# Kernel optimization log

Hardware: AMD Instinct MI355X
Metric: run time of the kernel (lower is better)

## Reference

```python
import jax, jax.numpy as jnp
import numpy as np

HEADS = 8
DIM_HEAD = 64


def setup_inputs() -> dict:
    key = jax.random.key(0)
    k1, k2, k3 = jax.random.split(key, 3)
    dim = 512
    hidden = HEADS * DIM_HEAD  # 512
    x = jax.random.normal(k1, (16, dim, 64, 64), dtype=jnp.float32)
    # 1x1 convs expressed as dense matrices (out_ch, in_ch)
    w_qkv = jax.random.normal(k2, (3 * hidden, dim), dtype=jnp.float32) * (1.0 / np.sqrt(dim))
    w_out = jax.random.normal(k3, (dim, hidden), dtype=jnp.float32) * (1.0 / np.sqrt(hidden))
    b_out = jnp.zeros((dim,), dtype=jnp.float32)
    return {"x": x, "w_qkv": w_qkv, "w_out": w_out, "b_out": b_out}


def reference(x, w_qkv, w_out, b_out):
    b, c, h, w = x.shape
    hw = h * w
    # 1x1 conv == channel matmul: (b, 3*hidden, hw)
    xf = x.reshape(b, c, hw)
    qkv = jnp.einsum('oc,bcn->bon', w_qkv, xf)
    # split into q,k,v each (b, heads, dim_head, hw)
    qkv = qkv.reshape(b, 3, HEADS, DIM_HEAD, hw)
    q, k, v = qkv[:, 0], qkv[:, 1], qkv[:, 2]
    k = jax.nn.softmax(k, axis=-1)  # softmax over spatial dim
    # context: (b, heads, dim_head, dim_head)
    context = jnp.einsum('bhcn,bhdn->bhcd', k, v)
    # out: context^T @ q -> (b, heads, dim_head, hw)
    out = jnp.einsum('bhcd,bhcn->bhdn', context, q)
    out = out.reshape(b, HEADS * DIM_HEAD, h, w)
    # to_out 1x1 conv with bias
    outf = out.reshape(b, HEADS * DIM_HEAD, hw)
    y = jnp.einsum('oc,bcn->bon', w_out, outf) + b_out[None, :, None]
    return y.reshape(b, -1, h, w)
```

## Files before the change

kernel.cpp:

```cpp
#include <hip/hip_runtime.h>
#include <string.h>

typedef __bf16 bf16x8 __attribute__((ext_vector_type(8)));
typedef float f32x4 __attribute__((ext_vector_type(4)));
typedef unsigned short u16;
typedef u16 u16x8 __attribute__((ext_vector_type(8)));

#define NB 16
#define CD 512
#define NN 4096
#define O3 1536

__device__ __forceinline__ u16 f2bf(float f) {
    union { float f; unsigned int u; } v; v.f = f;
    unsigned int r = v.u + 0x7fffu + ((v.u >> 16) & 1u);
    return (u16)(r >> 16);
}
__device__ __forceinline__ float bf2f(u16 s) {
    union { unsigned int u; float f; } v; v.u = ((unsigned int)s) << 16;
    return v.f;
}

__device__ __forceinline__ void gl2lds16(const u16* g, u16* l) {
    __builtin_amdgcn_global_load_lds(
        (const void __attribute__((address_space(1)))*)g,
        (void __attribute__((address_space(3)))*)l,
        16, 0, 0);
}

__global__ void k_convert(const float* __restrict__ in, u16* __restrict__ out, int n) {
    int i = blockIdx.x * 256 + threadIdx.x;
    if (i < n) out[i] = f2bf(in[i]);
}

__global__ __launch_bounds__(256) void k_transpose_x(const float* __restrict__ x,
                                                     u16* __restrict__ xt) {
    __shared__ float tile[64][65];
    const int b = blockIdx.y;
    const int ntile = blockIdx.x & 63;
    const int ctile = blockIdx.x >> 6;
    const int t = threadIdx.x;
    const int r = t >> 2;
    const int q = t & 3;

    const float* xb = x + ((size_t)b * CD + ctile * 64 + r) * NN + ntile * 64;
#pragma unroll
    for (int j = 0; j < 4; ++j) {
        float4 v = *(const float4*)&xb[q * 16 + j * 4];
        tile[r][q * 16 + j * 4 + 0] = v.x;
        tile[r][q * 16 + j * 4 + 1] = v.y;
        tile[r][q * 16 + j * 4 + 2] = v.z;
        tile[r][q * 16 + j * 4 + 3] = v.w;
    }
    __syncthreads();
    u16* xtb = xt + ((size_t)b * NN + ntile * 64 + r) * CD + ctile * 64 + q * 16;
    u16x8 o0, o1;
#pragma unroll
    for (int j = 0; j < 8; ++j) {
        o0[j] = f2bf(tile[q * 16 + j][r]);
        o1[j] = f2bf(tile[q * 16 + 8 + j][r]);
    }
    *(u16x8*)&xtb[0] = o0;
    *(u16x8*)&xtb[8] = o1;
}

__global__ __launch_bounds__(256, 2) void k_gemm1(
        const u16* __restrict__ A, const u16* __restrict__ Bt,
        u16* __restrict__ qt, u16* __restrict__ kbuf, u16* __restrict__ vbuf) {
    __shared__ __align__(16) u16 As[128 * 64];
    __shared__ __align__(16) u16 Bs[128 * 64];
    const int t = threadIdx.x;
    const int gid = blockIdx.x;
    const int xcd = gid & 7;
    const int j = gid >> 3;
    const int ot = j % 12;
    const int bn = (j / 12) * 8 + xcd;
    const int b = bn >> 5;
    const int nt = bn & 31;

    const int lane = t & 63, w = t >> 6;
    const int l15 = lane & 15, quad = lane >> 4;
    const int wm = (w >> 1) * 64, wn = (w & 1) * 64;
    const int srow = t >> 3;
    const int kc = (t & 7) * 8;

    const u16* Ab = A + (size_t)(ot * 128) * CD;
    const u16* Bb = Bt + (size_t)b * NN * CD + (size_t)(nt * 128) * CD;

    f32x4 acc[4][4] = {};

    for (int k0 = 0; k0 < CD; k0 += 64) {
        __syncthreads();
        gl2lds16(Ab + (size_t)(srow     ) * CD + k0 + kc, &As[t * 8]);
        gl2lds16(Ab + (size_t)(srow + 32) * CD + k0 + kc, &As[2048 + t * 8]);
        gl2lds16(Ab + (size_t)(srow + 64) * CD + k0 + kc, &As[4096 + t * 8]);
        gl2lds16(Ab + (size_t)(srow + 96) * CD + k0 + kc, &As[6144 + t * 8]);
        gl2lds16(Bb + (size_t)(srow     ) * CD + k0 + kc, &Bs[t * 8]);
        gl2lds16(Bb + (size_t)(srow + 32) * CD + k0 + kc, &Bs[2048 + t * 8]);
        gl2lds16(Bb + (size_t)(srow + 64) * CD + k0 + kc, &Bs[4096 + t * 8]);
        gl2lds16(Bb + (size_t)(srow + 96) * CD + k0 + kc, &Bs[6144 + t * 8]);
        __syncthreads();
#pragma unroll
        for (int h = 0; h < 2; ++h) {
            bf16x8 af[4], bfr[4];
#pragma unroll
            for (int mi = 0; mi < 4; ++mi)
                af[mi] = *(const bf16x8*)&As[(wm + mi * 16 + l15) * 64 + h * 32 + quad * 8];
#pragma unroll
            for (int ni = 0; ni < 4; ++ni)
                bfr[ni] = *(const bf16x8*)&Bs[(wn + ni * 16 + l15) * 64 + h * 32 + quad * 8];
#pragma unroll
            for (int mi = 0; mi < 4; ++mi)
#pragma unroll
                for (int ni = 0; ni < 4; ++ni)
                    acc[mi][ni] = __builtin_amdgcn_mfma_f32_16x16x32_bf16(
                        af[mi], bfr[ni], acc[mi][ni], 0, 0, 0);
        }
    }

    const int sec = ot >> 2;
    const int lrowbase = ot * 128 - sec * 512;
#pragma unroll
    for (int mi = 0; mi < 4; ++mi) {
        int lr = lrowbase + wm + mi * 16 + quad * 4;
#pragma unroll
        for (int ni = 0; ni < 4; ++ni) {
            int nc = nt * 128 + wn + ni * 16 + l15;
            if (sec == 0) {
                ushort4 pk;
                pk.x = f2bf(acc[mi][ni][0]); pk.y = f2bf(acc[mi][ni][1]);
                pk.z = f2bf(acc[mi][ni][2]); pk.w = f2bf(acc[mi][ni][3]);
                *(ushort4*)&qt[((size_t)b * NN + nc) * CD + lr] = pk;
            } else {
                u16* dst = (sec == 1) ? kbuf : vbuf;
#pragma unroll
                for (int r = 0; r < 4; ++r)
                    dst[((size_t)(b * 512 + lr + r)) * NN + nc] = f2bf(acc[mi][ni][r]);
            }
        }
    }
}

__global__ __launch_bounds__(256) void k_ctx(const u16* __restrict__ kbuf,
                                             const u16* __restrict__ vbuf,
                                             float* __restrict__ ctxT,
                                             float* __restrict__ lsum) {
    const int bh = blockIdx.y;
    const int chunk = blockIdx.x;
    const int t = threadIdx.x, lane = t & 63, w = t >> 6;
    const int l15 = lane & 15, quad = lane >> 4;
    const int cb = w * 16;

    const u16* krow = kbuf + (size_t)(bh * 64 + cb + l15) * NN;
    const u16* vb   = vbuf + (size_t)bh * 64 * NN;

    f32x4 acc[4] = {};
    float ls = 0.f;
    for (int i = 0; i < 32; ++i) {
        int n0 = chunk * 1024 + i * 32 + quad * 8;
        u16x8 ku = *(const u16x8*)&krow[n0];
        u16x8 afu;
#pragma unroll
        for (int jj = 0; jj < 8; ++jj) {
            float ev = __expf(fminf(bf2f(ku[jj]), 30.f));
            ls += ev;
            afu[jj] = f2bf(ev);
        }
        bf16x8 af = __builtin_bit_cast(bf16x8, afu);
#pragma unroll
        for (int di = 0; di < 4; ++di) {
            bf16x8 bfv = *(const bf16x8*)&vb[(size_t)(di * 16 + l15) * NN + n0];
            acc[di] = __builtin_amdgcn_mfma_f32_16x16x32_bf16(af, bfv, acc[di], 0, 0, 0);
        }
    }
    ls += __shfl_xor(ls, 16);
    ls += __shfl_xor(ls, 32);
    if (quad == 0) atomicAdd(&lsum[(size_t)bh * 64 + cb + l15], ls);

    const int c = cb + quad * 4;
#pragma unroll
    for (int di = 0; di < 4; ++di) {
        int d = di * 16 + l15;
#pragma unroll
        for (int r = 0; r < 4; ++r)
            atomicAdd(&ctxT[((size_t)bh * 64 + d) * 64 + c + r], acc[di][r]);
    }
}

__global__ __launch_bounds__(256) void k_weff(const float* __restrict__ wout,
                                              const float* __restrict__ ctxT,
                                              const float* __restrict__ lsum,
                                              u16* __restrict__ weff) {
    int idx = blockIdx.x * 256 + threadIdx.x;
    int b = idx >> 18;
    int o = (idx >> 9) & 511;
    int hc = idx & 511;
    int h = hc >> 6, c = hc & 63;
    const float* wr = wout + o * 512 + h * 64;
    const float* cr = ctxT + ((size_t)b * 8 + h) * 4096 + c;
    float s = 0.f;
#pragma unroll
    for (int d = 0; d < 64; ++d) s += wr[d] * cr[d * 64];
    s *= 1.0f / lsum[((size_t)b * 8 + h) * 64 + c];
    weff[idx] = f2bf(s);
}

__global__ __launch_bounds__(256, 2) void k_gemm2(
        const u16* __restrict__ weff, const u16* __restrict__ qt,
        const float* __restrict__ bout, float* __restrict__ y) {
    __shared__ __align__(16) u16 As[128 * 64];
    __shared__ __align__(16) u16 Bs[128 * 64];
    const int t = threadIdx.x;
    const int gid = blockIdx.x;
    const int xcd = gid & 7;
    const int j = gid >> 3;
    const int ot = j & 3;
    const int bn = (j >> 2) * 8 + xcd;
    const int b = bn >> 5;
    const int nt = bn & 31;

    const int lane = t & 63, w = t >> 6;
    const int l15 = lane & 15, quad = lane >> 4;
    const int wm = (w >> 1) * 64, wn = (w & 1) * 64;
    const int srow = t >> 3;
    const int kc = (t & 7) * 8;

    const u16* Ab = weff + (size_t)b * 512 * 512 + (size_t)(ot * 128) * CD;
    const u16* Bb = qt + (size_t)b * NN * CD + (size_t)(nt * 128) * CD;

    f32x4 acc[4][4] = {};

    for (int k0 = 0; k0 < CD; k0 += 64) {
        __syncthreads();
        gl2lds16(Ab + (size_t)(srow     ) * CD + k0 + kc, &As[t * 8]);
        gl2lds16(Ab + (size_t)(srow + 32) * CD + k0 + kc, &As[2048 + t * 8]);
        gl2lds16(Ab + (size_t)(srow + 64) * CD + k0 + kc, &As[4096 + t * 8]);
        gl2lds16(Ab + (size_t)(srow + 96) * CD + k0 + kc, &As[6144 + t * 8]);
        gl2lds16(Bb + (size_t)(srow     ) * CD + k0 + kc, &Bs[t * 8]);
        gl2lds16(Bb + (size_t)(srow + 32) * CD + k0 + kc, &Bs[2048 + t * 8]);
        gl2lds16(Bb + (size_t)(srow + 64) * CD + k0 + kc, &Bs[4096 + t * 8]);
        gl2lds16(Bb + (size_t)(srow + 96) * CD + k0 + kc, &Bs[6144 + t * 8]);
        __syncthreads();
#pragma unroll
        for (int h = 0; h < 2; ++h) {
            bf16x8 af[4], bfr[4];
#pragma unroll
            for (int mi = 0; mi < 4; ++mi)
                af[mi] = *(const bf16x8*)&As[(wm + mi * 16 + l15) * 64 + h * 32 + quad * 8];
#pragma unroll
            for (int ni = 0; ni < 4; ++ni)
                bfr[ni] = *(const bf16x8*)&Bs[(wn + ni * 16 + l15) * 64 + h * 32 + quad * 8];
#pragma unroll
            for (int mi = 0; mi < 4; ++mi)
#pragma unroll
                for (int ni = 0; ni < 4; ++ni)
                    acc[mi][ni] = __builtin_amdgcn_mfma_f32_16x16x32_bf16(
                        af[mi], bfr[ni], acc[mi][ni], 0, 0, 0);
        }
    }

#pragma unroll
    for (int mi = 0; mi < 4; ++mi) {
        int o = ot * 128 + wm + mi * 16 + quad * 4;
#pragma unroll
        for (int ni = 0; ni < 4; ++ni) {
            int nc = nt * 128 + wn + ni * 16 + l15;
#pragma unroll
            for (int r = 0; r < 4; ++r)
                y[((size_t)(b * 512 + o + r)) * NN + nc] = acc[mi][ni][r] + bout[o + r];
        }
    }
}

extern "C" void kernel_launch(void* const* d_in, const int* in_sizes, int n_in,
                              void* d_out, int out_size, void* d_ws, size_t ws_size,
                              hipStream_t stream) {
    const float* x    = (const float*)d_in[0];
    const float* wqkv = (const float*)d_in[1];
    const float* wout = (const float*)d_in[2];
    const float* bout = (const float*)d_in[3];
    float* y = (float*)d_out;

    char* ws = (char*)d_ws;
    u16*   xt   = (u16*)(ws);
    u16*   wqb  = (u16*)(ws + 67108864);
    u16*   qt   = (u16*)(ws + 68681728);
    u16*   kbuf = (u16*)(ws + 135790592);
    u16*   vbuf = (u16*)(ws + 202899456);
    float* ctxT = (float*)(ws + 270008320);
    float* lsum = (float*)(ws + 272105472);
    u16*   weff = (u16*)(ws + 272138240);

    hipMemsetAsync(ctxT, 0, 2097152 + 32768, stream);

    k_convert<<<(O3 * CD + 255) / 256, 256, 0, stream>>>(wqkv, wqb, O3 * CD);
    k_transpose_x<<<dim3(64 * 8, NB), 256, 0, stream>>>(x, xt);
    k_gemm1<<<12 * 32 * NB, 256, 0, stream>>>(wqb, xt, qt, kbuf, vbuf);
    k_ctx<<<dim3(4, NB * 8), 256, 0, stream>>>(kbuf, vbuf, ctxT, lsum);
    k_weff<<<(NB * 512 * 512) / 256, 256, 0, stream>>>(wout, ctxT, lsum, weff);
    k_gemm2<<<4 * 32 * NB, 256, 0, stream>>>(weff, qt, bout, y);
}
```

Measured before the change: 538.6 us.

## Rewrite both GEMMs as 256x256 tiles with double-buffered swizzled LDS pipeline

Both projection GEMMs move from 128x128 tiles with a single LDS buffer and two full syncs per k-step to a shared 256x256-tile core with 8 waves. The core double-buffers LDS, prefetches the next k-slices in quarter chunks interleaved with MFMA groups, XOR-swizzles the LDS layout to avoid bank conflicts, and raises wave priority during MFMA. The block-to-XCD mapping is also reworked for L2 locality. The aim is to hide global-load latency and cut LDS traffic per flop, at the cost of 128KB of LDS per block, more registers, and fragile hand-placed waitcnt and barrier logic.

```diff
diff --git a/kernel.cpp b/kernel.cpp
--- a/kernel.cpp
+++ b/kernel.cpp
@@ -64,78 +64,149 @@
     *(u16x8*)&xtb[8] = o1;
 }
 
-__global__ __launch_bounds__(256, 2) void k_gemm1(
+
+__device__ __forceinline__ void lda8(const u16* p, bf16x8 (&aa)[4][2],
+                                     int aoff, int sw0, int sw1) {
+#pragma unroll
+    for (int mi = 0; mi < 4; ++mi) {
+        aa[mi][0] = *(const bf16x8*)&p[aoff + mi * 1024 + sw0];
+        aa[mi][1] = *(const bf16x8*)&p[aoff + mi * 1024 + sw1];
+    }
+}
+
+__device__ __forceinline__ void ldb4(const u16* p, bf16x8 (&bb)[2][2],
+                                     int boff, int sw0, int sw1) {
+#pragma unroll
+    for (int ni = 0; ni < 2; ++ni) {
+        bb[ni][0] = *(const bf16x8*)&p[boff + ni * 1024 + sw0];
+        bb[ni][1] = *(const bf16x8*)&p[boff + ni * 1024 + sw1];
+    }
+}
+
+__device__ __forceinline__ void mfma16(bf16x8 (&aa)[4][2], bf16x8 (&bb)[2][2],
+                                       f32x4 (&ac)[4][2]) {
+    __builtin_amdgcn_s_setprio(1);
+#pragma unroll
+    for (int mi = 0; mi < 4; ++mi)
+#pragma unroll
+        for (int ni = 0; ni < 2; ++ni) {
+            ac[mi][ni] = __builtin_amdgcn_mfma_f32_16x16x32_bf16(
+                aa[mi][0], bb[ni][0], ac[mi][ni], 0, 0, 0);
+            ac[mi][ni] = __builtin_amdgcn_mfma_f32_16x16x32_bf16(
+                aa[mi][1], bb[ni][1], ac[mi][ni], 0, 0, 0);
+        }
+    __builtin_amdgcn_s_setprio(0);
+}
+
+#define MIDBAR() do { \
+    asm volatile("" ::: "memory"); \
+    __builtin_amdgcn_s_barrier(); \
+    asm volatile("s_waitcnt lgkmcnt(0)" ::: "memory"); \
+} while (0)
+
+#define ENDBAR() do { \
+    asm volatile("" ::: "memory"); \
+    __builtin_amdgcn_s_barrier(); \
+    asm volatile("" ::: "memory"); \
+} while (0)
+
+__device__ __forceinline__ void gemm256_core(const u16* __restrict__ Abase,
+                                             const u16* __restrict__ Bbase,
+                                             f32x4 (&acc)[2][2][4][2]) {
+    __shared__ __align__(16) u16 lds[2][2][2][8192];
+
+    const int t = threadIdx.x;
+    const int lane = t & 63;
+    const int w = t >> 6;
+    const int l15 = lane & 15, quad = lane >> 4;
+    const int r0 = t >> 3;
+    const int sg = ((t & 7) ^ (r0 & 7)) * 8;
+    const int aoff = ((w >> 2) * 64 + l15) * 64;
+    const int boff = ((w & 3) * 32 + l15) * 64;
+    const int sw0 = ((0 + quad) ^ (l15 & 7)) * 8;
+    const int sw1 = ((4 + quad) ^ (l15 & 7)) * 8;
+
+    auto stage = [&](int op, int half, int tau) {
+        const u16* s = (op ? Bbase : Abase)
+                       + (size_t)(half * 128 + r0) * CD + tau * 64 + sg;
+        u16* d = &lds[tau & 1][op][half][t * 8];
+        gl2lds16(s, d);
+        gl2lds16(s + (size_t)64 * CD, d + 4096);
+    };
+
+    stage(0, 0, 0); stage(1, 0, 0); stage(1, 1, 0); stage(0, 1, 0);
+    stage(0, 0, 1); stage(1, 0, 1);
+    asm volatile("s_waitcnt vmcnt(4)" ::: "memory");
+    ENDBAR();
+
+    bf16x8 aa[4][2], bb0[2][2], bb1[2][2];
+    for (int kt = 0; kt < 8; ++kt) {
+        const int s = kt & 1;
+        lda8(&lds[s][0][0][0], aa, aoff, sw0, sw1);
+        ldb4(&lds[s][1][0][0], bb0, boff, sw0, sw1);
+        if (kt <= 6) stage(1, 1, kt + 1);
+        MIDBAR();
+        mfma16(aa, bb0, acc[0][0]);
+        ENDBAR();
+        ldb4(&lds[s][1][1][0], bb1, boff, sw0, sw1);
+        if (kt <= 6) stage(0, 1, kt + 1);
+        MIDBAR();
+        mfma16(aa, bb1, acc[0][1]);
+        ENDBAR();
+        lda8(&lds[s][0][1][0], aa, aoff, sw0, sw1);
+        if (kt <= 5) stage(0, 0, kt + 2);
+        MIDBAR();
+        mfma16(aa, bb0, acc[1][0]);
+        ENDBAR();
+        if (kt <= 5) stage(1, 0, kt + 2);
+        MIDBAR();
+        mfma16(aa, bb1, acc[1][1]);
+        if (kt == 6)      asm volatile("s_waitcnt vmcnt(0)" ::: "memory");
+        else if (kt < 6)  asm volatile("s_waitcnt vmcnt(4)" ::: "memory");
+        ENDBAR();
+    }
+}
+
+__global__ __launch_bounds__(512, 2) void k_gemm1(
         const u16* __restrict__ A, const u16* __restrict__ Bt,
         u16* __restrict__ qt, u16* __restrict__ kbuf, u16* __restrict__ vbuf) {
-    __shared__ __align__(16) u16 As[128 * 64];
-    __shared__ __align__(16) u16 Bs[128 * 64];
+    const int gid = blockIdx.x;
+    const int u = (gid & 7) * 192 + (gid >> 3);
+    const int mt = u % 6;
+    const int bn = u / 6;
+    const int b = bn >> 4;
+    const int nt = bn & 15;
     const int t = threadIdx.x;
-    const int gid = blockIdx.x;
-    const int xcd = gid & 7;
-    const int j = gid >> 3;
-    const int ot = j % 12;
-    const int bn = (j / 12) * 8 + xcd;
-    const int b = bn >> 5;
-    const int nt = bn & 31;
-
     const int lane = t & 63, w = t >> 6;
     const int l15 = lane & 15, quad = lane >> 4;
-    const int wm = (w >> 1) * 64, wn = (w & 1) * 64;
-    const int srow = t >> 3;
-    const int kc = (t & 7) * 8;
-
-    const u16* Ab = A + (size_t)(ot * 128) * CD;
-    const u16* Bb = Bt + (size_t)b * NN * CD + (size_t)(nt * 128) * CD;
-
-    f32x4 acc[4][4] = {};
-
-    for (int k0 = 0; k0 < CD; k0 += 64) {
-        __syncthreads();
-        gl2lds16(Ab + (size_t)(srow     ) * CD + k0 + kc, &As[t * 8]);
-        gl2lds16(Ab + (size_t)(srow + 32) * CD + k0 + kc, &As[2048 + t * 8]);
-        gl2lds16(Ab + (size_t)(srow + 64) * CD + k0 + kc, &As[4096 + t * 8]);
-        gl2lds16(Ab + (size_t)(srow + 96) * CD + k0 + kc, &As[6144 + t * 8]);
-        gl2lds16(Bb + (size_t)(srow     ) * CD + k0 + kc, &Bs[t * 8]);
-        gl2lds16(Bb + (size_t)(srow + 32) * CD + k0 + kc, &Bs[2048 + t * 8]);
-        gl2lds16(Bb + (size_t)(srow + 64) * CD + k0 + kc, &Bs[4096 + t * 8]);
-        gl2lds16(Bb + (size_t)(srow + 96) * CD + k0 + kc, &Bs[6144 + t * 8]);
-        __syncthreads();
-#pragma unroll
-        for (int h = 0; h < 2; ++h) {
-            bf16x8 af[4], bfr[4];
-#pragma unroll
-            for (int mi = 0; mi < 4; ++mi)
-                af[mi] = *(const bf16x8*)&As[(wm + mi * 16 + l15) * 64 + h * 32 + quad * 8];
-#pragma unroll
-            for (int ni = 0; ni < 4; ++ni)
-                bfr[ni] = *(const bf16x8*)&Bs[(wn + ni * 16 + l15) * 64 + h * 32 + quad * 8];
-#pragma unroll
-            for (int mi = 0; mi < 4; ++mi)
-#pragma unroll
-                for (int ni = 0; ni < 4; ++ni)
-                    acc[mi][ni] = __builtin_amdgcn_mfma_f32_16x16x32_bf16(
-                        af[mi], bfr[ni], acc[mi][ni], 0, 0, 0);
-        }
-    }
-
-    const int sec = ot >> 2;
-    const int lrowbase = ot * 128 - sec * 512;
+
+    f32x4 acc[2][2][4][2] = {};
+    gemm256_core(A + (size_t)(mt * 256) * CD,
+                 Bt + ((size_t)b * NN + nt * 256) * CD, acc);
+
+    const int sec = mt >> 1;
+    const int lrb = mt * 256 - sec * 512;
+#pragma unroll
+    for (int qm = 0; qm < 2; ++qm)
 #pragma unroll
     for (int mi = 0; mi < 4; ++mi) {
-        int lr = lrowbase + wm + mi * 16 + quad * 4;
-#pragma unroll
-        for (int ni = 0; ni < 4; ++ni) {
-            int nc = nt * 128 + wn + ni * 16 + l15;
+        const int ml = qm * 128 + (w >> 2) * 64 + mi * 16 + quad * 4;
+#pragma unroll
+        for (int qn = 0; qn < 2; ++qn)
+#pragma unroll
+        for (int ni = 0; ni < 2; ++ni) {
+            const int n = nt * 256 + qn * 128 + (w & 3) * 32 + ni * 16 + l15;
+            f32x4 v = acc[qm][qn][mi][ni];
             if (sec == 0) {
                 ushort4 pk;
-                pk.x = f2bf(acc[mi][ni][0]); pk.y = f2bf(acc[mi][ni][1]);
-                pk.z = f2bf(acc[mi][ni][2]); pk.w = f2bf(acc[mi][ni][3]);
-                *(ushort4*)&qt[((size_t)b * NN + nc) * CD + lr] = pk;
+                pk.x = f2bf(v[0]); pk.y = f2bf(v[1]);
+                pk.z = f2bf(v[2]); pk.w = f2bf(v[3]);
+                *(ushort4*)&qt[((size_t)b * NN + n) * CD + mt * 256 + ml] = pk;
             } else {
                 u16* dst = (sec == 1) ? kbuf : vbuf;
 #pragma unroll
                 for (int r = 0; r < 4; ++r)
-                    dst[((size_t)(b * 512 + lr + r)) * NN + nc] = f2bf(acc[mi][ni][r]);
+                    dst[((size_t)(b * 512 + lrb + ml + r)) * NN + n] = f2bf(v[r]);
             }
         }
     }
@@ -205,69 +276,37 @@
     weff[idx] = f2bf(s);
 }
 
-__global__ __launch_bounds__(256, 2) void k_gemm2(
+__global__ __launch_bounds__(512, 2) void k_gemm2(
         const u16* __restrict__ weff, const u16* __restrict__ qt,
         const float* __restrict__ bout, float* __restrict__ y) {
-    __shared__ __align__(16) u16 As[128 * 64];
-    __shared__ __align__(16) u16 Bs[128 * 64];
+    const int gid = blockIdx.x;
+    const int u = (gid & 7) * 64 + (gid >> 3);
+    const int mt = u & 1;
+    const int bn = u >> 1;
+    const int b = bn >> 4;
+    const int nt = bn & 15;
     const int t = threadIdx.x;
-    const int gid = blockIdx.x;
-    const int xcd = gid & 7;
-    const int j = gid >> 3;
-    const int ot = j & 3;
-    const int bn = (j >> 2) * 8 + xcd;
-    const int b = bn >> 5;
-    const int nt = bn & 31;
-
     const int lane = t & 63, w = t >> 6;
     const int l15 = lane & 15, quad = lane >> 4;
-    const int wm = (w >> 1) * 64, wn = (w & 1) * 64;
-    const int srow = t >> 3;
-    const int kc = (t & 7) * 8;
-
-    const u16* Ab = weff + (size_t)b * 512 * 512 + (size_t)(ot * 128) * CD;
-    const u16* Bb = qt + (size_t)b * NN * CD + (size_t)(nt * 128) * CD;
-
-    f32x4 acc[4][4] = {};
-
-    for (int k0 = 0; k0 < CD; k0 += 64) {
-        __syncthreads();
-        gl2lds16(Ab + (size_t)(srow     ) * CD + k0 + kc, &As[t * 8]);
-        gl2lds16(Ab + (size_t)(srow + 32) * CD + k0 + kc, &As[2048 + t * 8]);
-        gl2lds16(Ab + (size_t)(srow + 64) * CD + k0 + kc, &As[4096 + t * 8]);
-        gl2lds16(Ab + (size_t)(srow + 96) * CD + k0 + kc, &As[6144 + t * 8]);
-        gl2lds16(Bb + (size_t)(srow     ) * CD + k0 + kc, &Bs[t * 8]);
-        gl2lds16(Bb + (size_t)(srow + 32) * CD + k0 + kc, &Bs[2048 + t * 8]);
-        gl2lds16(Bb + (size_t)(srow + 64) * CD + k0 + kc, &Bs[4096 + t * 8]);
-        gl2lds16(Bb + (size_t)(srow + 96) * CD + k0 + kc, &Bs[6144 + t * 8]);
-        __syncthreads();
-#pragma unroll
-        for (int h = 0; h < 2; ++h) {
-            bf16x8 af[4], bfr[4];
-#pragma unroll
-            for (int mi = 0; mi < 4; ++mi)
-                af[mi] = *(const bf16x8*)&As[(wm + mi * 16 + l15) * 64 + h * 32 + quad * 8];
-#pragma unroll
-            for (int ni = 0; ni < 4; ++ni)
-                bfr[ni] = *(const bf16x8*)&Bs[(wn + ni * 16 + l15) * 64 + h * 32 + quad * 8];
-#pragma unroll
-            for (int mi = 0; mi < 4; ++mi)
-#pragma unroll
-                for (int ni = 0; ni < 4; ++ni)
-                    acc[mi][ni] = __builtin_amdgcn_mfma_f32_16x16x32_bf16(
-                        af[mi], bfr[ni], acc[mi][ni], 0, 0, 0);
-        }
-    }
-
+
+    f32x4 acc[2][2][4][2] = {};
+    gemm256_core(weff + (size_t)b * 512 * 512 + (size_t)(mt * 256) * CD,
+                 qt + ((size_t)b * NN + nt * 256) * CD, acc);
+
+#pragma unroll
+    for (int qm = 0; qm < 2; ++qm)
 #pragma unroll
     for (int mi = 0; mi < 4; ++mi) {
-        int o = ot * 128 + wm + mi * 16 + quad * 4;
-#pragma unroll
-        for (int ni = 0; ni < 4; ++ni) {
-            int nc = nt * 128 + wn + ni * 16 + l15;
+        const int o = mt * 256 + qm * 128 + (w >> 2) * 64 + mi * 16 + quad * 4;
+#pragma unroll
+        for (int qn = 0; qn < 2; ++qn)
+#pragma unroll
+        for (int ni = 0; ni < 2; ++ni) {
+            const int n = nt * 256 + qn * 128 + (w & 3) * 32 + ni * 16 + l15;
+            f32x4 v = acc[qm][qn][mi][ni];
 #pragma unroll
             for (int r = 0; r < 4; ++r)
-                y[((size_t)(b * 512 + o + r)) * NN + nc] = acc[mi][ni][r] + bout[o + r];
+                y[((size_t)(b * 512 + o + r)) * NN + n] = v[r] + bout[o + r];
         }
     }
 }
@@ -295,8 +334,8 @@
 
     k_convert<<<(O3 * CD + 255) / 256, 256, 0, stream>>>(wqkv, wqb, O3 * CD);
     k_transpose_x<<<dim3(64 * 8, NB), 256, 0, stream>>>(x, xt);
-    k_gemm1<<<12 * 32 * NB, 256, 0, stream>>>(wqb, xt, qt, kbuf, vbuf);
+    k_gemm1<<<1536, 512, 0, stream>>>(wqb, xt, qt, kbuf, vbuf);
     k_ctx<<<dim3(4, NB * 8), 256, 0, stream>>>(kbuf, vbuf, ctxT, lsum);
     k_weff<<<(NB * 512 * 512) / 256, 256, 0, stream>>>(wout, ctxT, lsum, weff);
-    k_gemm2<<<4 * 32 * NB, 256, 0, stream>>>(weff, qt, bout, y);
-}
+    k_gemm2<<<512, 512, 0, stream>>>(weff, qt, bout, y);
+}
```

Measured after the change: 523.8 us. 2.7% less time.
